# Kernel tuning notes

Hardware: AMD Instinct MI355X
Metric: run time of the kernel (lower is better)

Reference implementation:

```python
import jax, jax.numpy as jnp
import numpy as np

TAU = 1.0
REDUCTION = 'mean'


def setup_inputs() -> dict:
    key = jax.random.key(0)
    k1, k2 = jax.random.split(key)
    n, d, n_classes = 8192, 128, 100
    projection = jax.random.normal(k1, (n, d), dtype=jnp.float32)
    y = jax.random.randint(k2, (n,), 0, n_classes, dtype=jnp.int64)
    return {"projection": projection, "y": y}


def reference(projection, y):
    n = projection.shape[0]
    sim = projection @ projection.T  # [n, n]
    eq = y[:, None] == y[None, :]
    same_mask = eq & ~jnp.eye(n, dtype=bool)  # same class, excluding self
    diff_mask = ~eq

    big = jnp.asarray(jnp.inf, dtype=sim.dtype)
    # masked per-row min over same-class sims (0 if row has none)
    min_same = jnp.min(jnp.where(same_mask, sim, big), axis=1)
    min_same = jnp.where(jnp.any(same_mask, axis=1), min_same, 0.0)
    # masked per-row max over diff-class sims (0 if row has none)
    max_diff = jnp.max(jnp.where(diff_mask, sim, -big), axis=1)
    max_diff = jnp.where(jnp.any(diff_mask, axis=1), max_diff, 0.0)

    loss_i = jnp.maximum(0.0, min_same + max_diff + TAU)  # [n]
    if REDUCTION == 'mean':
        return jnp.mean(loss_i)
    return jnp.sum(loss_i)
```

## Files before the change

### kernel.cpp

```cpp
#include <hip/hip_runtime.h>
#include <hip/hip_bf16.h>
#include <float.h>

#define N 8192
#define D 128
#define BM 128
#define BN 64
#define GY 16
#define COLS_PER_BLOCK (N / GY)
#define TILES (COLS_PER_BLOCK / BN)
#define NPART GY
#define LOSS_BLOCKS (N / 256)

typedef unsigned short u16;
typedef unsigned int u32;
typedef __attribute__((ext_vector_type(8))) short bf16x8;
typedef __attribute__((ext_vector_type(4))) float f32x4;

typedef const __attribute__((address_space(1))) u32 glb_u32;
typedef __attribute__((address_space(3))) u32 lds_u32;

__device__ inline u16 f32_to_bf16_rtne(float f) {
  union { float f; unsigned int u; } c; c.f = f;
  unsigned int u = c.u;
  u += 0x7FFFu + ((u >> 16) & 1u);
  return (u16)(u >> 16);
}

__global__ __launch_bounds__(256) void convert_kernel(const float* __restrict__ P,
                                                      u16* __restrict__ Pb) {
  int i = blockIdx.x * 256 + threadIdx.x;
  float4 v = reinterpret_cast<const float4*>(P)[i];
  uint2 o;
  o.x = (unsigned)f32_to_bf16_rtne(v.x) | ((unsigned)f32_to_bf16_rtne(v.y) << 16);
  o.y = (unsigned)f32_to_bf16_rtne(v.z) | ((unsigned)f32_to_bf16_rtne(v.w) << 16);
  reinterpret_cast<uint2*>(Pb)[i] = o;
}

__global__ __launch_bounds__(256) void margin_main(const u16* __restrict__ Pb,
                                                   const int* __restrict__ y,
                                                   float* __restrict__ pmin,
                                                   float* __restrict__ pmax) {
  __shared__ __align__(16) char ldsB[2][BN * 256];
  __shared__ int ldsY[2][BN];

  const int tid  = threadIdx.x;
  const int w    = tid >> 6;
  const int lane = tid & 63;
  const int c15  = lane & 15;
  const int g    = lane >> 4;

  const int R0 = blockIdx.x * BM;
  const int C0 = blockIdx.y * COLS_PER_BLOCK;
  const char* pbb = (const char*)Pb;

  bf16x8 afrag[2][4];
#pragma unroll
  for (int rg = 0; rg < 2; ++rg) {
    const char* ap = pbb + (size_t)(R0 + w * 32 + rg * 16 + c15) * 256 + g * 16;
#pragma unroll
    for (int kk = 0; kk < 4; ++kk)
      afrag[rg][kk] = *reinterpret_cast<const bf16x8*>(ap + kk * 64);
  }

  int rowI[2][4], yrow[2][4];
#pragma unroll
  for (int rg = 0; rg < 2; ++rg)
#pragma unroll
    for (int r = 0; r < 4; ++r) {
      rowI[rg][r] = R0 + w * 32 + rg * 16 + g * 4 + r;
      yrow[rg][r] = y[rowI[rg][r]];
    }

  float mins[2][4], maxd[2][4];
#pragma unroll
  for (int rg = 0; rg < 2; ++rg)
#pragma unroll
    for (int r = 0; r < 4; ++r) { mins[rg][r] = FLT_MAX; maxd[rg][r] = -FLT_MAX; }

  auto STAGE = [&](int buf, int t) {
    const char* gb = pbb + (size_t)(C0 + t * BN) * 256;
#pragma unroll
    for (int j = 0; j < 4; ++j) {
      const int L = ((w * 4 + j) * 64 + lane) * 16;
      const int c = L >> 8;
      const int o = L & 255;
      const int src = c * 256 + (o ^ ((c & 15) << 4));
      char* ldst = &ldsB[buf][(w * 4 + j) * 1024];
      __builtin_amdgcn_global_load_lds((glb_u32*)(gb + src), (lds_u32*)ldst, 16, 0, 0);
    }
    if (w == 0)
      __builtin_amdgcn_global_load_lds((glb_u32*)(y + C0 + t * BN + lane),
                                       (lds_u32*)&ldsY[buf][0], 4, 0, 0);
  };

  STAGE(0, 0);

  for (int t = 0; t < TILES; ++t) {
    const int buf = t & 1;
    asm volatile("s_waitcnt vmcnt(0)" ::: "memory");
    __syncthreads();
    if (t + 1 < TILES) STAGE(buf ^ 1, t + 1);

    const char* Bb = &ldsB[buf][0];
    const int ct0 = C0 + t * BN;
#pragma unroll
    for (int s = 0; s < 4; ++s) {
      const int c = s * 16 + c15;
      bf16x8 bf[4];
#pragma unroll
      for (int kk = 0; kk < 4; ++kk) {
        const int off = c * 256 + (((g * 16) | (kk * 64)) ^ (c15 << 4));
        bf[kk] = *reinterpret_cast<const bf16x8*>(Bb + off);
      }
      f32x4 acc0 = {0.f, 0.f, 0.f, 0.f}, acc1 = {0.f, 0.f, 0.f, 0.f};
#pragma unroll
      for (int kk = 0; kk < 4; ++kk) {
        acc0 = __builtin_amdgcn_mfma_f32_16x16x32_bf16(afrag[0][kk], bf[kk], acc0, 0, 0, 0);
        acc1 = __builtin_amdgcn_mfma_f32_16x16x32_bf16(afrag[1][kk], bf[kk], acc1, 0, 0, 0);
      }
      const int col  = ct0 + c;
      const int ycol = ldsY[buf][c];
#pragma unroll
      for (int r = 0; r < 4; ++r) {
        {
          const float v = acc0[r];
          if (ycol == yrow[0][r]) {
            if (col != rowI[0][r]) mins[0][r] = fminf(mins[0][r], v);
          } else maxd[0][r] = fmaxf(maxd[0][r], v);
        }
        {
          const float v = acc1[r];
          if (ycol == yrow[1][r]) {
            if (col != rowI[1][r]) mins[1][r] = fminf(mins[1][r], v);
          } else maxd[1][r] = fmaxf(maxd[1][r], v);
        }
      }
    }
    __syncthreads();
  }

#pragma unroll
  for (int off = 1; off < 16; off <<= 1)
#pragma unroll
    for (int rg = 0; rg < 2; ++rg)
#pragma unroll
      for (int r = 0; r < 4; ++r) {
        mins[rg][r] = fminf(mins[rg][r], __shfl_xor(mins[rg][r], off, 64));
        maxd[rg][r] = fmaxf(maxd[rg][r], __shfl_xor(maxd[rg][r], off, 64));
      }

  if (c15 == 0) {
#pragma unroll
    for (int rg = 0; rg < 2; ++rg)
#pragma unroll
      for (int r = 0; r < 4; ++r) {
        pmin[(size_t)blockIdx.y * N + rowI[rg][r]] = mins[rg][r];
        pmax[(size_t)blockIdx.y * N + rowI[rg][r]] = maxd[rg][r];
      }
  }
}

__global__ __launch_bounds__(256) void loss_kernel(const float* __restrict__ pmin,
                                                   const float* __restrict__ pmax,
                                                   float* __restrict__ blockSums) {
  const int row = blockIdx.x * 256 + threadIdx.x;
  float mn = FLT_MAX, mx = -FLT_MAX;
#pragma unroll
  for (int s = 0; s < NPART; ++s) {
    mn = fminf(mn, pmin[(size_t)s * N + row]);
    mx = fmaxf(mx, pmax[(size_t)s * N + row]);
  }
  if (mn == FLT_MAX)  mn = 0.f;
  if (mx == -FLT_MAX) mx = 0.f;
  float loss = fmaxf(0.f, mn + mx + 1.0f);

#pragma unroll
  for (int off = 32; off >= 1; off >>= 1)
    loss += __shfl_down(loss, off, 64);
  __shared__ float wsum[4];
  if ((threadIdx.x & 63) == 0) wsum[threadIdx.x >> 6] = loss;
  __syncthreads();
  if (threadIdx.x == 0)
    blockSums[blockIdx.x] = wsum[0] + wsum[1] + wsum[2] + wsum[3];
}

__global__ __launch_bounds__(64) void finalize_kernel(const float* __restrict__ blockSums,
                                                      float* __restrict__ out) {
  float v = (threadIdx.x < LOSS_BLOCKS) ? blockSums[threadIdx.x] : 0.f;
#pragma unroll
  for (int off = 32; off >= 1; off >>= 1)
    v += __shfl_down(v, off, 64);
  if (threadIdx.x == 0) out[0] = v / (float)N;
}

extern "C" void kernel_launch(void* const* d_in, const int* in_sizes, int n_in,
                              void* d_out, int out_size, void* d_ws, size_t ws_size,
                              hipStream_t stream) {
  const float* P = (const float*)d_in[0];
  const int*   y = (const int*)d_in[1];
  float* out = (float*)d_out;

  u16*   Pb        = (u16*)d_ws;
  float* pmin      = (float*)((char*)d_ws + (size_t)N * D * sizeof(u16));
  float* pmax      = pmin + (size_t)N * NPART;
  float* blockSums = pmax + (size_t)N * NPART;

  convert_kernel<<<dim3(N * D / 4 / 256), 256, 0, stream>>>(P, Pb);
  margin_main<<<dim3(N / BM, GY), 256, 0, stream>>>(Pb, y, pmin, pmax);
  loss_kernel<<<dim3(LOSS_BLOCKS), 256, 0, stream>>>(pmin, pmax, blockSums);
  finalize_kernel<<<1, 64, 0, stream>>>(blockSums, out);
}
```

Baseline: 47.32 us.

## Double row tile, triple-buffer B with one barrier, specialize diagonal blocks

Raises the row tile from 128 to 256, so each wave keeps four 16-row A fragment groups and each staged B tile feeds twice as many MFMAs. B tiles move from double to triple buffering, with a counted vmcnt wait and a single barrier per tile in place of two __syncthreads. All column labels for the block are loaded into LDS once up front. A template flag drops the self-exclusion check on blocks that cannot touch the diagonal, and the per-element masked min/max becomes branchless selects. The trade-offs are higher register pressure (launch bounds request 2 blocks per SM) and half as many blocks in the grid.

Result: faster. 38.56 us (-18.5%).

```diff
diff --git a/kernel.cpp b/kernel.cpp
--- a/kernel.cpp
+++ b/kernel.cpp
@@ -4,7 +4,7 @@
 
 #define N 8192
 #define D 128
-#define BM 128
+#define BM 256
 #define BN 64
 #define GY 16
 #define COLS_PER_BLOCK (N / GY)
@@ -37,73 +37,76 @@
   reinterpret_cast<uint2*>(Pb)[i] = o;
 }
 
-__global__ __launch_bounds__(256) void margin_main(const u16* __restrict__ Pb,
-                                                   const int* __restrict__ y,
-                                                   float* __restrict__ pmin,
-                                                   float* __restrict__ pmax) {
-  __shared__ __align__(16) char ldsB[2][BN * 256];
-  __shared__ int ldsY[2][BN];
-
+template <bool DIAG>
+__device__ __forceinline__ void pipeline(const char* __restrict__ pbb,
+                                         const int* __restrict__ y,
+                                         float* __restrict__ pmin,
+                                         float* __restrict__ pmax,
+                                         char* ldsB, int* ldsY,
+                                         int R0, int C0, int slot) {
   const int tid  = threadIdx.x;
   const int w    = tid >> 6;
   const int lane = tid & 63;
   const int c15  = lane & 15;
   const int g    = lane >> 4;
 
-  const int R0 = blockIdx.x * BM;
-  const int C0 = blockIdx.y * COLS_PER_BLOCK;
-  const char* pbb = (const char*)Pb;
-
-  bf16x8 afrag[2][4];
-#pragma unroll
-  for (int rg = 0; rg < 2; ++rg) {
-    const char* ap = pbb + (size_t)(R0 + w * 32 + rg * 16 + c15) * 256 + g * 16;
-#pragma unroll
-    for (int kk = 0; kk < 4; ++kk)
-      afrag[rg][kk] = *reinterpret_cast<const bf16x8*>(ap + kk * 64);
-  }
-
-  int rowI[2][4], yrow[2][4];
-#pragma unroll
-  for (int rg = 0; rg < 2; ++rg)
-#pragma unroll
-    for (int r = 0; r < 4; ++r) {
-      rowI[rg][r] = R0 + w * 32 + rg * 16 + g * 4 + r;
-      yrow[rg][r] = y[rowI[rg][r]];
-    }
-
-  float mins[2][4], maxd[2][4];
-#pragma unroll
-  for (int rg = 0; rg < 2; ++rg)
-#pragma unroll
-    for (int r = 0; r < 4; ++r) { mins[rg][r] = FLT_MAX; maxd[rg][r] = -FLT_MAX; }
+  {
+    const int* gy = y + C0 + w * 128 + lane;
+    lds_u32* dst = (lds_u32*)(ldsY + w * 128);
+    __builtin_amdgcn_global_load_lds((glb_u32*)gy,        dst,      4, 0, 0);
+    __builtin_amdgcn_global_load_lds((glb_u32*)(gy + 64), dst + 64, 4, 0, 0);
+  }
 
   auto STAGE = [&](int buf, int t) {
     const char* gb = pbb + (size_t)(C0 + t * BN) * 256;
+    char* base = ldsB + buf * (BN * 256);
 #pragma unroll
     for (int j = 0; j < 4; ++j) {
       const int L = ((w * 4 + j) * 64 + lane) * 16;
       const int c = L >> 8;
       const int o = L & 255;
       const int src = c * 256 + (o ^ ((c & 15) << 4));
-      char* ldst = &ldsB[buf][(w * 4 + j) * 1024];
-      __builtin_amdgcn_global_load_lds((glb_u32*)(gb + src), (lds_u32*)ldst, 16, 0, 0);
+      __builtin_amdgcn_global_load_lds((glb_u32*)(gb + src),
+                                       (lds_u32*)(base + (w * 4 + j) * 1024), 16, 0, 0);
     }
-    if (w == 0)
-      __builtin_amdgcn_global_load_lds((glb_u32*)(y + C0 + t * BN + lane),
-                                       (lds_u32*)&ldsY[buf][0], 4, 0, 0);
   };
 
   STAGE(0, 0);
-
+  STAGE(1, 1);
+
+  bf16x8 afrag[4][4];
+#pragma unroll
+  for (int rg = 0; rg < 4; ++rg) {
+    const char* ap = pbb + (size_t)(R0 + w * 64 + rg * 16 + c15) * 256 + g * 16;
+#pragma unroll
+    for (int kk = 0; kk < 4; ++kk)
+      afrag[rg][kk] = *reinterpret_cast<const bf16x8*>(ap + kk * 64);
+  }
+
+  int rowI[4][4], yrow[4][4];
+#pragma unroll
+  for (int rg = 0; rg < 4; ++rg)
+#pragma unroll
+    for (int r = 0; r < 4; ++r) {
+      rowI[rg][r] = R0 + w * 64 + rg * 16 + g * 4 + r;
+      yrow[rg][r] = y[rowI[rg][r]];
+    }
+
+  float mins[4][4], maxd[4][4];
+#pragma unroll
+  for (int rg = 0; rg < 4; ++rg)
+#pragma unroll
+    for (int r = 0; r < 4; ++r) { mins[rg][r] = FLT_MAX; maxd[rg][r] = -FLT_MAX; }
+
+#pragma unroll 1
   for (int t = 0; t < TILES; ++t) {
-    const int buf = t & 1;
-    asm volatile("s_waitcnt vmcnt(0)" ::: "memory");
-    __syncthreads();
-    if (t + 1 < TILES) STAGE(buf ^ 1, t + 1);
-
-    const char* Bb = &ldsB[buf][0];
-    const int ct0 = C0 + t * BN;
+    if (t + 1 < TILES) asm volatile("s_waitcnt vmcnt(4)" ::: "memory");
+    else               asm volatile("s_waitcnt vmcnt(0)" ::: "memory");
+    __builtin_amdgcn_s_barrier();
+    if (t + 2 < TILES) STAGE((t + 2) % 3, t + 2);
+
+    const char* Bb = ldsB + (t % 3) * (BN * 256);
+    const int ct0 = t * BN;
 #pragma unroll
     for (int s = 0; s < 4; ++s) {
       const int c = s * 16 + c15;
@@ -113,37 +116,38 @@
         const int off = c * 256 + (((g * 16) | (kk * 64)) ^ (c15 << 4));
         bf[kk] = *reinterpret_cast<const bf16x8*>(Bb + off);
       }
-      f32x4 acc0 = {0.f, 0.f, 0.f, 0.f}, acc1 = {0.f, 0.f, 0.f, 0.f};
-#pragma unroll
-      for (int kk = 0; kk < 4; ++kk) {
-        acc0 = __builtin_amdgcn_mfma_f32_16x16x32_bf16(afrag[0][kk], bf[kk], acc0, 0, 0, 0);
-        acc1 = __builtin_amdgcn_mfma_f32_16x16x32_bf16(afrag[1][kk], bf[kk], acc1, 0, 0, 0);
-      }
-      const int col  = ct0 + c;
-      const int ycol = ldsY[buf][c];
-#pragma unroll
-      for (int r = 0; r < 4; ++r) {
-        {
-          const float v = acc0[r];
-          if (ycol == yrow[0][r]) {
-            if (col != rowI[0][r]) mins[0][r] = fminf(mins[0][r], v);
-          } else maxd[0][r] = fmaxf(maxd[0][r], v);
+      f32x4 acc[4];
+#pragma unroll
+      for (int rg = 0; rg < 4; ++rg) acc[rg] = (f32x4){0.f, 0.f, 0.f, 0.f};
+#pragma unroll
+      for (int kk = 0; kk < 4; ++kk)
+#pragma unroll
+        for (int rg = 0; rg < 4; ++rg)
+          acc[rg] = __builtin_amdgcn_mfma_f32_16x16x32_bf16(afrag[rg][kk], bf[kk],
+                                                            acc[rg], 0, 0, 0);
+      const int colB = ct0 + c;
+      const int col  = C0 + colB;
+      const int ycol = ldsY[colB];
+#pragma unroll
+      for (int rg = 0; rg < 4; ++rg)
+#pragma unroll
+        for (int r = 0; r < 4; ++r) {
+          const float v = acc[rg][r];
+          const bool same = (ycol == yrow[rg][r]);
+          bool okmin = same;
+          if (DIAG) okmin = same && (col != rowI[rg][r]);
+          const float cmin = okmin ? v : FLT_MAX;
+          const float cmax = same ? -FLT_MAX : v;
+          mins[rg][r] = fminf(mins[rg][r], cmin);
+          maxd[rg][r] = fmaxf(maxd[rg][r], cmax);
         }
-        {
-          const float v = acc1[r];
-          if (ycol == yrow[1][r]) {
-            if (col != rowI[1][r]) mins[1][r] = fminf(mins[1][r], v);
-          } else maxd[1][r] = fmaxf(maxd[1][r], v);
-        }
-      }
     }
-    __syncthreads();
   }
 
 #pragma unroll
   for (int off = 1; off < 16; off <<= 1)
 #pragma unroll
-    for (int rg = 0; rg < 2; ++rg)
+    for (int rg = 0; rg < 4; ++rg)
 #pragma unroll
       for (int r = 0; r < 4; ++r) {
         mins[rg][r] = fminf(mins[rg][r], __shfl_xor(mins[rg][r], off, 64));
@@ -152,13 +156,27 @@
 
   if (c15 == 0) {
 #pragma unroll
-    for (int rg = 0; rg < 2; ++rg)
+    for (int rg = 0; rg < 4; ++rg)
 #pragma unroll
       for (int r = 0; r < 4; ++r) {
-        pmin[(size_t)blockIdx.y * N + rowI[rg][r]] = mins[rg][r];
-        pmax[(size_t)blockIdx.y * N + rowI[rg][r]] = maxd[rg][r];
+        pmin[(size_t)slot * N + rowI[rg][r]] = mins[rg][r];
+        pmax[(size_t)slot * N + rowI[rg][r]] = maxd[rg][r];
       }
   }
+}
+
+__global__ __launch_bounds__(256, 2) void margin_main(const u16* __restrict__ Pb,
+                                                      const int* __restrict__ y,
+                                                      float* __restrict__ pmin,
+                                                      float* __restrict__ pmax) {
+  __shared__ __align__(16) char ldsB[3][BN * 256];
+  __shared__ int ldsY[COLS_PER_BLOCK];
+  const int R0 = blockIdx.x * BM;
+  const int C0 = blockIdx.y * COLS_PER_BLOCK;
+  if ((unsigned)(R0 - C0) < (unsigned)COLS_PER_BLOCK)
+    pipeline<true>((const char*)Pb, y, pmin, pmax, &ldsB[0][0], ldsY, R0, C0, blockIdx.y);
+  else
+    pipeline<false>((const char*)Pb, y, pmin, pmax, &ldsB[0][0], ldsY, R0, C0, blockIdx.y);
 }
 
 __global__ __launch_bounds__(256) void loss_kernel(const float* __restrict__ pmin,
```

## Exploit Gram matrix symmetry with triangular tiles and atomic min/max reduction

Applied to the files above, without the earlier changes.

Computes only the upper-triangular 128x128 tiles of the similarity matrix and uses each off-diagonal tile for both its row and its column reductions. Per-row and per-column min/max results are merged through atomicMin/atomicMax on order-preserving uint encodings, which replaces the 16-way partial buffers. The aim is to roughly halve the MFMA work and shrink the loss kernel's reads. In exchange it adds global atomics, a per-block column reduction through LDS, and smaller single-tile blocks with no double-buffered pipeline.

Result: slower. 100.1 us (+111.6%).

```diff
diff --git a/kernel.cpp b/kernel.cpp
--- a/kernel.cpp
+++ b/kernel.cpp
@@ -4,12 +4,9 @@
 
 #define N 8192
 #define D 128
-#define BM 128
-#define BN 64
-#define GY 16
-#define COLS_PER_BLOCK (N / GY)
-#define TILES (COLS_PER_BLOCK / BN)
-#define NPART GY
+#define BS 128
+#define NB (N / BS)
+#define TRI_BLOCKS (NB * (NB + 1) / 2)
 #define LOSS_BLOCKS (N / 256)
 
 typedef unsigned short u16;
@@ -20,93 +17,109 @@
 typedef const __attribute__((address_space(1))) u32 glb_u32;
 typedef __attribute__((address_space(3))) u32 lds_u32;
 
-__device__ inline u16 f32_to_bf16_rtne(float f) {
-  union { float f; unsigned int u; } c; c.f = f;
-  unsigned int u = c.u;
+__device__ __forceinline__ u32 fmap(float x) {
+  u32 u = __float_as_uint(x);
+  return (u >> 31) ? ~u : (u | 0x80000000u);
+}
+__device__ __forceinline__ float funmap(u32 m) {
+  u32 u = (m & 0x80000000u) ? (m ^ 0x80000000u) : ~m;
+  return __uint_as_float(u);
+}
+#define SENT_MIN 0xFF7FFFFFu
+#define SENT_MAX 0x00800000u
+
+__device__ __forceinline__ u16 f32_to_bf16_rtne(float f) {
+  u32 u = __float_as_uint(f);
   u += 0x7FFFu + ((u >> 16) & 1u);
   return (u16)(u >> 16);
 }
 
 __global__ __launch_bounds__(256) void convert_kernel(const float* __restrict__ P,
-                                                      u16* __restrict__ Pb) {
+                                                      u16* __restrict__ Pb,
+                                                      u32* __restrict__ pminU,
+                                                      u32* __restrict__ pmaxU) {
   int i = blockIdx.x * 256 + threadIdx.x;
   float4 v = reinterpret_cast<const float4*>(P)[i];
   uint2 o;
   o.x = (unsigned)f32_to_bf16_rtne(v.x) | ((unsigned)f32_to_bf16_rtne(v.y) << 16);
   o.y = (unsigned)f32_to_bf16_rtne(v.z) | ((unsigned)f32_to_bf16_rtne(v.w) << 16);
   reinterpret_cast<uint2*>(Pb)[i] = o;
-}
-
-__global__ __launch_bounds__(256) void margin_main(const u16* __restrict__ Pb,
-                                                   const int* __restrict__ y,
-                                                   float* __restrict__ pmin,
-                                                   float* __restrict__ pmax) {
-  __shared__ __align__(16) char ldsB[2][BN * 256];
-  __shared__ int ldsY[2][BN];
-
+  if (blockIdx.x < 32) {
+    int k = blockIdx.x * 256 + threadIdx.x;
+    pminU[k] = SENT_MIN;
+    pmaxU[k] = SENT_MAX;
+  }
+}
+
+template <bool DIAG>
+__device__ __forceinline__ void marginBody(const char* __restrict__ pbb,
+                                           const int* __restrict__ y,
+                                           u32* __restrict__ pminU,
+                                           u32* __restrict__ pmaxU,
+                                           char* ldsB, int* ldsY,
+                                           float* ldsColMin, float* ldsColMax,
+                                           int R0, int C0) {
   const int tid  = threadIdx.x;
   const int w    = tid >> 6;
   const int lane = tid & 63;
   const int c15  = lane & 15;
   const int g    = lane >> 4;
 
-  const int R0 = blockIdx.x * BM;
-  const int C0 = blockIdx.y * COLS_PER_BLOCK;
-  const char* pbb = (const char*)Pb;
-
-  bf16x8 afrag[2][4];
-#pragma unroll
-  for (int rg = 0; rg < 2; ++rg) {
-    const char* ap = pbb + (size_t)(R0 + w * 32 + rg * 16 + c15) * 256 + g * 16;
-#pragma unroll
-    for (int kk = 0; kk < 4; ++kk)
-      afrag[rg][kk] = *reinterpret_cast<const bf16x8*>(ap + kk * 64);
-  }
-
-  int rowI[2][4], yrow[2][4];
-#pragma unroll
-  for (int rg = 0; rg < 2; ++rg)
-#pragma unroll
-    for (int r = 0; r < 4; ++r) {
-      rowI[rg][r] = R0 + w * 32 + rg * 16 + g * 4 + r;
-      yrow[rg][r] = y[rowI[rg][r]];
-    }
-
-  float mins[2][4], maxd[2][4];
-#pragma unroll
-  for (int rg = 0; rg < 2; ++rg)
-#pragma unroll
-    for (int r = 0; r < 4; ++r) { mins[rg][r] = FLT_MAX; maxd[rg][r] = -FLT_MAX; }
-
-  auto STAGE = [&](int buf, int t) {
-    const char* gb = pbb + (size_t)(C0 + t * BN) * 256;
+#pragma unroll
+  for (int t = 0; t < 2; ++t) {
+    const char* gb = pbb + (size_t)(C0 + t * 64) * 256;
+    char* base = ldsB + t * (64 * 256);
 #pragma unroll
     for (int j = 0; j < 4; ++j) {
       const int L = ((w * 4 + j) * 64 + lane) * 16;
       const int c = L >> 8;
       const int o = L & 255;
       const int src = c * 256 + (o ^ ((c & 15) << 4));
-      char* ldst = &ldsB[buf][(w * 4 + j) * 1024];
-      __builtin_amdgcn_global_load_lds((glb_u32*)(gb + src), (lds_u32*)ldst, 16, 0, 0);
+      __builtin_amdgcn_global_load_lds((glb_u32*)(gb + src),
+                                       (lds_u32*)(base + (w * 4 + j) * 1024), 16, 0, 0);
     }
-    if (w == 0)
-      __builtin_amdgcn_global_load_lds((glb_u32*)(y + C0 + t * BN + lane),
-                                       (lds_u32*)&ldsY[buf][0], 4, 0, 0);
-  };
-
-  STAGE(0, 0);
-
-  for (int t = 0; t < TILES; ++t) {
-    const int buf = t & 1;
-    asm volatile("s_waitcnt vmcnt(0)" ::: "memory");
-    __syncthreads();
-    if (t + 1 < TILES) STAGE(buf ^ 1, t + 1);
-
-    const char* Bb = &ldsB[buf][0];
-    const int ct0 = C0 + t * BN;
+  }
+  {
+    const int* gy = y + C0 + lane;
+    lds_u32* dst = (lds_u32*)(ldsY + w * 128);
+    __builtin_amdgcn_global_load_lds((glb_u32*)gy,        dst,      4, 0, 0);
+    __builtin_amdgcn_global_load_lds((glb_u32*)(gy + 64), dst + 64, 4, 0, 0);
+  }
+
+  const int rowbase = R0 + w * 32 + g * 4;
+
+  bf16x8 afrag[2][4];
+#pragma unroll
+  for (int rg = 0; rg < 2; ++rg) {
+    const char* ap = pbb + (size_t)(R0 + w * 32 + rg * 16 + c15) * 256 + g * 16;
+#pragma unroll
+    for (int kk = 0; kk < 4; ++kk)
+      afrag[rg][kk] = *reinterpret_cast<const bf16x8*>(ap + kk * 64);
+  }
+
+  int yrow[2][4];
+#pragma unroll
+  for (int rg = 0; rg < 2; ++rg)
+#pragma unroll
+    for (int r = 0; r < 4; ++r)
+      yrow[rg][r] = y[rowbase + rg * 16 + r];
+
+  float rmin[2][4], rmax[2][4];
+#pragma unroll
+  for (int rg = 0; rg < 2; ++rg)
+#pragma unroll
+    for (int r = 0; r < 4; ++r) { rmin[rg][r] = FLT_MAX; rmax[rg][r] = -FLT_MAX; }
+
+  __syncthreads();
+
+  int* myY = ldsY + w * 128;
+#pragma unroll
+  for (int t = 0; t < 2; ++t) {
+    const char* Bb = ldsB + t * (64 * 256);
 #pragma unroll
     for (int s = 0; s < 4; ++s) {
       const int c = s * 16 + c15;
+      const int colB = t * 64 + c;
       bf16x8 bf[4];
 #pragma unroll
       for (int kk = 0; kk < 4; ++kk) {
@@ -114,65 +127,115 @@
         bf[kk] = *reinterpret_cast<const bf16x8*>(Bb + off);
       }
       f32x4 acc0 = {0.f, 0.f, 0.f, 0.f}, acc1 = {0.f, 0.f, 0.f, 0.f};
+      __builtin_amdgcn_s_setprio(1);
 #pragma unroll
       for (int kk = 0; kk < 4; ++kk) {
         acc0 = __builtin_amdgcn_mfma_f32_16x16x32_bf16(afrag[0][kk], bf[kk], acc0, 0, 0, 0);
         acc1 = __builtin_amdgcn_mfma_f32_16x16x32_bf16(afrag[1][kk], bf[kk], acc1, 0, 0, 0);
       }
-      const int col  = ct0 + c;
-      const int ycol = ldsY[buf][c];
+      __builtin_amdgcn_s_setprio(0);
+
+      const int ycol = myY[colB];
+      const int colg = C0 + colB;
+      float cmn = FLT_MAX, cmx = -FLT_MAX;
+#pragma unroll
+      for (int rg = 0; rg < 2; ++rg)
+#pragma unroll
+        for (int r = 0; r < 4; ++r) {
+          const float v = (rg == 0) ? acc0[r] : acc1[r];
+          const bool same = (ycol == yrow[rg][r]);
+          bool okmin = same;
+          if (DIAG) okmin = same && (colg != rowbase + rg * 16 + r);
+          const float cnd_min = okmin ? v : FLT_MAX;
+          const float cnd_max = same ? -FLT_MAX : v;
+          rmin[rg][r] = fminf(rmin[rg][r], cnd_min);
+          rmax[rg][r] = fmaxf(rmax[rg][r], cnd_max);
+          if (!DIAG) {
+            cmn = fminf(cmn, cnd_min);
+            cmx = fmaxf(cmx, cnd_max);
+          }
+        }
+      if (!DIAG) {
+        cmn = fminf(cmn, __shfl_xor(cmn, 16, 64));
+        cmn = fminf(cmn, __shfl_xor(cmn, 32, 64));
+        cmx = fmaxf(cmx, __shfl_xor(cmx, 16, 64));
+        cmx = fmaxf(cmx, __shfl_xor(cmx, 32, 64));
+        if (g == 0) {
+          ldsColMin[w * 128 + colB] = cmn;
+          ldsColMax[w * 128 + colB] = cmx;
+        }
+      }
+    }
+  }
+
+#pragma unroll
+  for (int off = 1; off < 16; off <<= 1)
+#pragma unroll
+    for (int rg = 0; rg < 2; ++rg)
 #pragma unroll
       for (int r = 0; r < 4; ++r) {
-        {
-          const float v = acc0[r];
-          if (ycol == yrow[0][r]) {
-            if (col != rowI[0][r]) mins[0][r] = fminf(mins[0][r], v);
-          } else maxd[0][r] = fmaxf(maxd[0][r], v);
-        }
-        {
-          const float v = acc1[r];
-          if (ycol == yrow[1][r]) {
-            if (col != rowI[1][r]) mins[1][r] = fminf(mins[1][r], v);
-          } else maxd[1][r] = fmaxf(maxd[1][r], v);
-        }
-      }
+        rmin[rg][r] = fminf(rmin[rg][r], __shfl_xor(rmin[rg][r], off, 64));
+        rmax[rg][r] = fmaxf(rmax[rg][r], __shfl_xor(rmax[rg][r], off, 64));
+      }
+  if (c15 == 0) {
+#pragma unroll
+    for (int rg = 0; rg < 2; ++rg)
+#pragma unroll
+      for (int r = 0; r < 4; ++r) {
+        const int row = rowbase + rg * 16 + r;
+        atomicMin(&pminU[row], fmap(rmin[rg][r]));
+        atomicMax(&pmaxU[row], fmap(rmax[rg][r]));
+      }
+  }
+
+  if (!DIAG) {
+    __syncthreads();
+    const int col   = tid & 127;
+    const int which = tid >> 7;
+    if (which == 0) {
+      float v = fminf(fminf(ldsColMin[col], ldsColMin[128 + col]),
+                      fminf(ldsColMin[256 + col], ldsColMin[384 + col]));
+      atomicMin(&pminU[C0 + col], fmap(v));
+    } else {
+      float v = fmaxf(fmaxf(ldsColMax[col], ldsColMax[128 + col]),
+                      fmaxf(ldsColMax[256 + col], ldsColMax[384 + col]));
+      atomicMax(&pmaxU[C0 + col], fmap(v));
     }
-    __syncthreads();
-  }
-
-#pragma unroll
-  for (int off = 1; off < 16; off <<= 1)
-#pragma unroll
-    for (int rg = 0; rg < 2; ++rg)
-#pragma unroll
-      for (int r = 0; r < 4; ++r) {
-        mins[rg][r] = fminf(mins[rg][r], __shfl_xor(mins[rg][r], off, 64));
-        maxd[rg][r] = fmaxf(maxd[rg][r], __shfl_xor(maxd[rg][r], off, 64));
-      }
-
-  if (c15 == 0) {
-#pragma unroll
-    for (int rg = 0; rg < 2; ++rg)
-#pragma unroll
-      for (int r = 0; r < 4; ++r) {
-        pmin[(size_t)blockIdx.y * N + rowI[rg][r]] = mins[rg][r];
-        pmax[(size_t)blockIdx.y * N + rowI[rg][r]] = maxd[rg][r];
-      }
-  }
-}
-
-__global__ __launch_bounds__(256) void loss_kernel(const float* __restrict__ pmin,
-                                                   const float* __restrict__ pmax,
+  }
+}
+
+__global__ __launch_bounds__(256, 4) void margin_main(const u16* __restrict__ Pb,
+                                                      const int* __restrict__ y,
+                                                      u32* __restrict__ pminU,
+                                                      u32* __restrict__ pmaxU) {
+  __shared__ __align__(16) char ldsB[2][64 * 256];
+  __shared__ int   ldsY[4 * 128];
+  __shared__ float ldsColMin[4 * 128];
+  __shared__ float ldsColMax[4 * 128];
+
+  const int t = blockIdx.x;
+  int i = (int)((129.0f - sqrtf((float)(16641 - 8 * t))) * 0.5f);
+  i = max(0, min(NB - 1, i));
+  while (i * NB - i * (i - 1) / 2 > t) --i;
+  while ((i + 1) * NB - (i + 1) * i / 2 <= t) ++i;
+  const int j = i + (t - (i * NB - i * (i - 1) / 2));
+
+  const int R0 = i * BS, C0 = j * BS;
+  if (i == j)
+    marginBody<true >((const char*)Pb, y, pminU, pmaxU, &ldsB[0][0], ldsY,
+                      ldsColMin, ldsColMax, R0, C0);
+  else
+    marginBody<false>((const char*)Pb, y, pminU, pmaxU, &ldsB[0][0], ldsY,
+                      ldsColMin, ldsColMax, R0, C0);
+}
+
+__global__ __launch_bounds__(256) void loss_kernel(const u32* __restrict__ pminU,
+                                                   const u32* __restrict__ pmaxU,
                                                    float* __restrict__ blockSums) {
   const int row = blockIdx.x * 256 + threadIdx.x;
-  float mn = FLT_MAX, mx = -FLT_MAX;
-#pragma unroll
-  for (int s = 0; s < NPART; ++s) {
-    mn = fminf(mn, pmin[(size_t)s * N + row]);
-    mx = fmaxf(mx, pmax[(size_t)s * N + row]);
-  }
-  if (mn == FLT_MAX)  mn = 0.f;
-  if (mx == -FLT_MAX) mx = 0.f;
+  const u32 um = pminU[row], ux = pmaxU[row];
+  const float mn = (um == SENT_MIN) ? 0.f : funmap(um);
+  const float mx = (ux == SENT_MAX) ? 0.f : funmap(ux);
   float loss = fmaxf(0.f, mn + mx + 1.0f);
 
 #pragma unroll
@@ -201,13 +264,13 @@
   const int*   y = (const int*)d_in[1];
   float* out = (float*)d_out;
 
-  u16*   Pb        = (u16*)d_ws;
-  float* pmin      = (float*)((char*)d_ws + (size_t)N * D * sizeof(u16));
-  float* pmax      = pmin + (size_t)N * NPART;
-  float* blockSums = pmax + (size_t)N * NPART;
-
-  convert_kernel<<<dim3(N * D / 4 / 256), 256, 0, stream>>>(P, Pb);
-  margin_main<<<dim3(N / BM, GY), 256, 0, stream>>>(Pb, y, pmin, pmax);
-  loss_kernel<<<dim3(LOSS_BLOCKS), 256, 0, stream>>>(pmin, pmax, blockSums);
+  u16* Pb        = (u16*)d_ws;
+  u32* pminU     = (u32*)((char*)d_ws + (size_t)N * D * sizeof(u16));
+  u32* pmaxU     = pminU + N;
+  float* blockSums = (float*)(pmaxU + N);
+
+  convert_kernel<<<dim3(N * D / 4 / 256), 256, 0, stream>>>(P, Pb, pminU, pmaxU);
+  margin_main<<<dim3(TRI_BLOCKS), 256, 0, stream>>>(Pb, y, pminU, pmaxU);
+  loss_kernel<<<dim3(LOSS_BLOCKS), 256, 0, stream>>>(pminU, pmaxU, blockSums);
   finalize_kernel<<<1, 64, 0, stream>>>(blockSums, out);
 }
```
